# Kernel tuning notes

Measured on AMD Instinct MI355X. Metric: run time of the kernel, lower is better.

The kernel has to match this reference:

```python
import jax, jax.numpy as jnp
import numpy as np

T, B = 50, 512
S, A, BEL, H, E, M = 256, 32, 1024, 1024, 1024, 256
MIN_STD = 0.1


def setup_inputs() -> dict:
    key = jax.random.key(0)
    ks = jax.random.split(key, 24)
    def rn(k, shape, scale=1.0):
        return jax.random.normal(k, shape, dtype=jnp.float32) * scale
    w = 0.05  # weight init scale
    return {
        "prev_state": rn(ks[0], (B, S)),
        "actions": rn(ks[1], (T, B, A)),
        "prev_belief": rn(ks[2], (B, BEL)),
        "observations": rn(ks[3], (T, B, E)),
        "nonterminals": jnp.ones((T, B, 1), dtype=jnp.float32),
        "map_embeddings": rn(ks[4], (T, B, M)),
        "map_embeddings_post": rn(ks[5], (T, B, M)),
        "noise_prior": rn(ks[6], (T, B, S)),
        "noise_post": rn(ks[7], (T, B, S)),
        "W_sa": rn(ks[8], (BEL, S + A + M), w), "b_sa": jnp.zeros((BEL,), jnp.float32),
        "W_ih": rn(ks[9], (3 * BEL, BEL), w), "b_ih": jnp.zeros((3 * BEL,), jnp.float32),
        "W_hh": rn(ks[10], (3 * BEL, BEL), w), "b_hh": jnp.zeros((3 * BEL,), jnp.float32),
        "W_bp": rn(ks[11], (H, BEL), w), "b_bp": jnp.zeros((H,), jnp.float32),
        "W_sp": rn(ks[12], (2 * S, H), w), "b_sp": jnp.zeros((2 * S,), jnp.float32),
        "W_bq": rn(ks[13], (H, BEL + E + M), w), "b_bq": jnp.zeros((H,), jnp.float32),
        "W_sq": rn(ks[14], (2 * S, H), w), "b_sq": jnp.zeros((2 * S,), jnp.float32),
    }


def reference(prev_state, actions, prev_belief, observations, nonterminals,
              map_embeddings, map_embeddings_post, noise_prior, noise_post,
              W_sa, b_sa, W_ih, b_ih, W_hh, b_hh,
              W_bp, b_bp, W_sp, b_sp, W_bq, b_bq, W_sq, b_sq):
    relu = jax.nn.relu
    def lin(x, W, b):
        return x @ W.T + b

    def gru(x, h):  # torch.nn.GRUCell math
        gi = x @ W_ih.T + b_ih
        gh = h @ W_hh.T + b_hh
        i_r, i_z, i_n = jnp.split(gi, 3, axis=1)
        h_r, h_z, h_n = jnp.split(gh, 3, axis=1)
        r = jax.nn.sigmoid(i_r + h_r)
        z = jax.nn.sigmoid(i_z + h_z)
        n = jnp.tanh(i_n + r * h_n)
        return (1.0 - z) * n + z * h

    def std(raw):
        return jnp.minimum(jax.nn.softplus(raw) + MIN_STD, 5.0)

    def step(carry, xs):
        belief, post_state = carry
        a, obs, nt, me, mp, np_, nq = xs
        s = post_state * nt
        hid = relu(lin(jnp.concatenate([s, a, me], axis=1), W_sa, b_sa))
        belief = gru(hid, belief)
        # prior p(z_t | h_t)
        hp = relu(lin(belief, W_bp, b_bp))
        p_mean, p_raw = jnp.split(lin(hp, W_sp, b_sp), 2, axis=1)
        p_std = std(p_raw)
        p_state = p_mean + p_std * np_
        # posterior q(z_t | h_t, e_t, m_t)
        hq = relu(lin(jnp.concatenate([belief, obs, mp], axis=1), W_bq, b_bq))
        q_mean, q_raw = jnp.split(lin(hq, W_sq, b_sq), 2, axis=1)
        q_std = std(q_raw)
        q_state = q_mean + q_std * nq
        return (belief, q_state), (belief, p_state, p_mean, p_std, q_state, q_mean, q_std)

    _, outs = jax.lax.scan(
        step, (prev_belief, prev_state),
        (actions, observations, nonterminals, map_embeddings,
         map_embeddings_post, noise_prior, noise_post))
    return outs  # 7 arrays, each (T, B, *)
```

## Files before the change

### kernel.cpp

```cpp
#include <hip/hip_runtime.h>
#include <hip/hip_bf16.h>

#define NT 50
#define NB 512
#define SD 256
#define BD 1024
#define HD 1024
#define ED 1024
#define MD 256
#define NBLK 512
#define PGSZ (1024 * 256)
#define K1BIG 0x40000000

typedef __attribute__((ext_vector_type(8))) short bf16x8;
typedef __attribute__((ext_vector_type(4))) float f32x4;

__device__ __forceinline__ void gload_lds16(const void* g, void* l) {
  __builtin_amdgcn_global_load_lds(
      (const __attribute__((address_space(1))) void*)g,
      (__attribute__((address_space(3))) void*)l, 16, 0, 0);
}

__device__ __forceinline__ void aload16(const void* a, f32x4* r) {
  asm volatile("global_load_dwordx4 %0, %1, off sc0" : "=&v"(*r) : "v"(a) : "memory");
}
__device__ __forceinline__ void aload4(const void* a, float* r) {
  asm volatile("global_load_dword %0, %1, off sc0" : "=&v"(*r) : "v"(a) : "memory");
}
#define VMWAIT(N)                                        \
  asm volatile("s_waitcnt vmcnt(" #N ")" ::: "memory");  \
  __builtin_amdgcn_sched_barrier(0);

__device__ __forceinline__ void astore16(void* g, f32x4 v) {
  asm volatile("global_store_dwordx4 %0, %1, off sc0" :: "v"(g), "v"(v) : "memory");
}
__device__ __forceinline__ void astore4(void* g, float v) {
  asm volatile("global_store_dword %0, %1, off sc0" :: "v"(g), "v"(v) : "memory");
}
__device__ __forceinline__ void astore2(void* g, unsigned v) {
  asm volatile("global_store_short %0, %1, off sc0" :: "v"(g), "v"(v) : "memory");
}
__device__ __forceinline__ void ntstore16(void* g, f32x4 v) {
  asm volatile("global_store_dwordx4 %0, %1, off nt" :: "v"(g), "v"(v) : "memory");
}
__device__ __forceinline__ void ntstore4(void* g, float v) {
  asm volatile("global_store_dword %0, %1, off nt" :: "v"(g), "v"(v) : "memory");
}

__device__ __forceinline__ float sigmoidf_(float x) { return 1.0f / (1.0f + __expf(-x)); }
__device__ __forceinline__ float softplusf_(float x) {
  return (x > 0.0f) ? (x + log1pf(__expf(-x))) : log1pf(__expf(x));
}
__device__ __forceinline__ unsigned short bfb(float x) {
  __hip_bfloat16 h = __float2bfloat16(x);
  return __builtin_bit_cast(unsigned short, h);
}

__device__ __forceinline__ void xbar(unsigned* cnt, int inst, int xcd, int nx) {
  asm volatile("s_waitcnt vmcnt(0) lgkmcnt(0)" ::: "memory");
  __syncthreads();
  if (threadIdx.x == 0) {
    unsigned* c = cnt + 256 + (size_t)(inst * 8 + xcd) * 16;
    __hip_atomic_fetch_add(c, 1u, __ATOMIC_RELAXED, __HIP_MEMORY_SCOPE_AGENT);
    while (__hip_atomic_load(c, __ATOMIC_RELAXED, __HIP_MEMORY_SCOPE_AGENT) < (unsigned)nx)
      __builtin_amdgcn_s_sleep(4);
  }
  __syncthreads();
}

__device__ __noinline__ void gemm64(
    int EPI, char* lds,
    const __hip_bfloat16* __restrict__ A1, int lda1,
    const __hip_bfloat16* __restrict__ A2, int lda2, int K1,
    const __hip_bfloat16* __restrict__ Wr, int ldw, int nIter,
    const float* __restrict__ bias, const float* __restrict__ Cadd,
    float* __restrict__ Cf, __hip_bfloat16* __restrict__ Cb, int ldc, int m0) {
  const int tid = threadIdx.x;
  const int lane = tid & 63, w = tid >> 6;
  const int wr = w >> 1, wc = w & 1;
  f32x4 acc[2][2] = {};
  const __hip_bfloat16* a1r = A1 + (size_t)(m0 + lane) * lda1;
  const __hip_bfloat16* a2r = A2 ? (A2 + (size_t)(m0 + lane) * lda2) : a1r;
  const __hip_bfloat16* wrow = Wr + (size_t)lane * ldw;

  f32x4 rA0, rA1;
  auto issueA = [&](int it) {
    const int k0 = it << 6;
    const __hip_bfloat16* as = (k0 < K1) ? (a1r + k0) : (a2r + (k0 - K1));
    aload16(as + (2 * w) * 8, &rA0);
    aload16(as + (2 * w + 1) * 8, &rA1);
  };
  auto writeA = [&](int it) {
    char* la = lds + ((it & 1) << 14);
    *(f32x4*)(la + (2 * w) * 1024 + lane * 16) = rA0;
    *(f32x4*)(la + (2 * w + 1) * 1024 + lane * 16) = rA1;
  };
  auto stageW = [&](int it) {
    const int k0 = it << 6;
    char* lb = lds + ((it & 1) << 14) + 8192;
    gload_lds16(wrow + k0 + (2 * w) * 8, lb + (2 * w) * 1024);
    gload_lds16(wrow + k0 + (2 * w + 1) * 8, lb + (2 * w + 1) * 1024);
  };

  __syncthreads();
  issueA(0);
  VMWAIT(0)
  writeA(0);
  stageW(0);

  const int kq = lane >> 4, r15 = lane & 15;
  for (int i = 0; i < nIter; ++i) {
    __syncthreads();
    if (i + 1 < nIter) {
      issueA(i + 1);
      stageW(i + 1);
    }
    const char* la = lds + ((i & 1) << 14);
    const char* lb = la + 8192;
#pragma unroll
    for (int s = 0; s < 2; ++s) {
      bf16x8 af[2], bfr[2];
#pragma unroll
      for (int m = 0; m < 2; ++m)
        af[m] = *(const bf16x8*)(la + (size_t)((s * 4 + kq) * 64 + wr * 32 + m * 16 + r15) * 16);
#pragma unroll
      for (int n = 0; n < 2; ++n)
        bfr[n] = *(const bf16x8*)(lb + (size_t)((s * 4 + kq) * 64 + wc * 32 + n * 16 + r15) * 16);
#pragma unroll
      for (int m = 0; m < 2; ++m)
#pragma unroll
        for (int n = 0; n < 2; ++n)
          acc[m][n] = __builtin_amdgcn_mfma_f32_16x16x32_bf16(af[m], bfr[n], acc[m][n], 0, 0, 0);
    }
    if (i + 1 < nIter) {
      VMWAIT(2)
      writeA(i + 1);
    }
  }

  const int rg = lane >> 4;
  float ad[2][2][4];
  if (EPI == 3) {
#pragma unroll
    for (int m = 0; m < 2; ++m)
#pragma unroll
      for (int n = 0; n < 2; ++n) {
        const int col = wc * 32 + n * 16 + r15;
#pragma unroll
        for (int i2 = 0; i2 < 4; ++i2) {
          const int row = m0 + wr * 32 + m * 16 + rg * 4 + i2;
          aload4(Cadd + (size_t)row * ldc + col, &ad[m][n][i2]);
        }
      }
    VMWAIT(0)
  }
#pragma unroll
  for (int m = 0; m < 2; ++m) {
#pragma unroll
    for (int n = 0; n < 2; ++n) {
      const int col = wc * 32 + n * 16 + r15;
      const float bv = bias ? bias[col] : 0.0f;
#pragma unroll
      for (int i2 = 0; i2 < 4; ++i2) {
        const int row = m0 + wr * 32 + m * 16 + rg * 4 + i2;
        float v = acc[m][n][i2] + bv;
        if (EPI == 3) v += ad[m][n][i2];
        if (EPI != 0) {
          v = v > 0.0f ? v : 0.0f;
          astore2(Cb + (size_t)row * ldc + col, (unsigned)bfb(v));
        } else {
          astore4(Cf + (size_t)row * ldc + col, v);
        }
      }
    }
  }
}

__device__ __noinline__ void gemm_head64(
    char* lds, const __hip_bfloat16* __restrict__ A,
    const __hip_bfloat16* __restrict__ Wr, const float* __restrict__ bias,
    const float* __restrict__ noise, float* __restrict__ st_o, float* __restrict__ mn_o,
    float* __restrict__ sd_o, const float* __restrict__ ntn,
    __hip_bfloat16* __restrict__ sprev, int isq, int n0, int m0) {
  const int tid = threadIdx.x;
  const int lane = tid & 63, w = tid >> 6;
  const int wr = w >> 1, wc = w & 1;
  f32x4 acc[2][2] = {};
  const __hip_bfloat16* ar = A + (size_t)(m0 + lane) * BD;
  const __hip_bfloat16* wrow = Wr + (size_t)lane * BD;

  f32x4 rA0, rA1;
  auto issueA = [&](int it) {
    const int k0 = it << 6;
    aload16(ar + k0 + (2 * w) * 8, &rA0);
    aload16(ar + k0 + (2 * w + 1) * 8, &rA1);
  };
  auto writeA = [&](int it) {
    char* la = lds + ((it & 1) << 14);
    *(f32x4*)(la + (2 * w) * 1024 + lane * 16) = rA0;
    *(f32x4*)(la + (2 * w + 1) * 1024 + lane * 16) = rA1;
  };
  auto stageW = [&](int it) {
    const int k0 = it << 6;
    char* lb = lds + ((it & 1) << 14) + 8192;
    gload_lds16(wrow + k0 + (2 * w) * 8, lb + (2 * w) * 1024);
    gload_lds16(wrow + k0 + (2 * w + 1) * 8, lb + (2 * w + 1) * 1024);
  };

  __syncthreads();
  issueA(0);
  VMWAIT(0)
  writeA(0);
  stageW(0);

  const int kq = lane >> 4, r15 = lane & 15;
  for (int i = 0; i < 16; ++i) {
    __syncthreads();
    if (i + 1 < 16) {
      issueA(i + 1);
      stageW(i + 1);
    }
    const char* la = lds + ((i & 1) << 14);
    const char* lb = la + 8192;
#pragma unroll
    for (int s = 0; s < 2; ++s) {
      bf16x8 af[2], bfr[2];
#pragma unroll
      for (int m = 0; m < 2; ++m)
        af[m] = *(const bf16x8*)(la + (size_t)((s * 4 + kq) * 64 + wr * 32 + m * 16 + r15) * 16);
#pragma unroll
      for (int n = 0; n < 2; ++n)
        bfr[n] = *(const bf16x8*)(lb + (size_t)((s * 4 + kq) * 64 + wc * 32 + n * 16 + r15) * 16);
#pragma unroll
      for (int m = 0; m < 2; ++m)
#pragma unroll
        for (int n = 0; n < 2; ++n)
          acc[m][n] = __builtin_amdgcn_mfma_f32_16x16x32_bf16(af[m], bfr[n], acc[m][n], 0, 0, 0);
    }
    if (i + 1 < 16) {
      VMWAIT(2)
      writeA(i + 1);
    }
  }

  const int rg = lane >> 4;
  const bool even = (r15 & 1) == 0;
#pragma unroll
  for (int m = 0; m < 2; ++m) {
#pragma unroll
    for (int n = 0; n < 2; ++n) {
      const int col = n0 + wc * 32 + n * 16 + r15;
      const int j = col >> 1;
      const float bv = bias[col];
#pragma unroll
      for (int i2 = 0; i2 < 4; ++i2) {
        const int row = m0 + wr * 32 + m * 16 + rg * 4 + i2;
        float v = acc[m][n][i2] + bv;
        float partner = __shfl_xor(v, 1);
        float mean = even ? v : partner;
        float raw = even ? partner : v;
        float sd = fminf(softplusf_(raw) + 0.1f, 5.0f);
        const size_t o = (size_t)row * SD + j;
        if (even) {
          float st = mean + sd * noise[o];
          ntstore4(mn_o + o, mean);
          ntstore4(st_o + o, st);
          if (isq) astore2(sprev + o, (unsigned)bfb(st * ntn[row]));
        } else {
          ntstore4(sd_o + o, sd);
        }
      }
    }
  }
}

struct Args {
  const float *prev_state, *actions, *prev_belief, *observations, *nonterminals,
      *me, *mp, *noise_p, *noise_q,
      *W_sa, *b_sa, *W_ih, *b_ih, *W_hh, *b_hh,
      *W_bp, *b_bp, *W_sp, *b_sp, *W_bq, *b_bq, *W_sq, *b_sq;
  float* out;
  unsigned* cnt;
  __hip_bfloat16 *Wsa, *Wih, *Whh, *Wbp, *Wbq, *Wsp, *Wsq;
  __hip_bfloat16 *actme, *obsmp, *sprev, *bel, *hid, *hpb, *hqb;
  float *gi, *gh, *hq_obs;
  float *bsp_ro, *bsq_ro;
};

__global__ __launch_bounds__(256) void prep(Args P) {
  const int gtid = blockIdx.x * 256 + threadIdx.x;
  for (int i = gtid; i < BD * 576; i += PGSZ) {
    int r = i / 576, k = i - r * 576;
    P.Wsa[i] = __float2bfloat16(k < 544 ? P.W_sa[(size_t)r * 544 + k] : 0.0f);
  }
  for (int i = gtid; i < 3 * BD * BD; i += PGSZ) P.Wih[i] = __float2bfloat16(P.W_ih[i]);
  for (int i = gtid; i < 3 * BD * BD; i += PGSZ) P.Whh[i] = __float2bfloat16(P.W_hh[i]);
  for (int i = gtid; i < HD * BD; i += PGSZ) P.Wbp[i] = __float2bfloat16(P.W_bp[i]);
  for (int i = gtid; i < HD * 2304; i += PGSZ) P.Wbq[i] = __float2bfloat16(P.W_bq[i]);
  for (int i = gtid; i < 512 * HD; i += PGSZ) {
    int r = i >> 10, k = i & 1023;
    int dr = (r < 256) ? (2 * r) : (2 * (r - 256) + 1);
    P.Wsp[(size_t)dr * 1024 + k] = __float2bfloat16(P.W_sp[i]);
    P.Wsq[(size_t)dr * 1024 + k] = __float2bfloat16(P.W_sq[i]);
  }
  for (int i = gtid; i < 512; i += PGSZ) {
    int dr = (i < 256) ? (2 * i) : (2 * (i - 256) + 1);
    P.bsp_ro[dr] = P.b_sp[i];
    P.bsq_ro[dr] = P.b_sq[i];
  }
  for (int i = gtid; i < NT * NB * 320; i += PGSZ) {
    int tb = i / 320, j = i - tb * 320;
    float v = (j < 32) ? P.actions[(size_t)tb * 32 + j]
                       : (j < 288 ? P.me[(size_t)tb * 256 + (j - 32)] : 0.0f);
    P.actme[i] = __float2bfloat16(v);
  }
  for (int i = gtid; i < NB * 1280; i += PGSZ) {
    int bb = i / 1280, j = i - bb * 1280;
    float v = (j < ED) ? P.observations[(size_t)bb * ED + j] : P.mp[(size_t)bb * MD + (j - ED)];
    P.obsmp[i] = __float2bfloat16(v);
  }
  for (int i = gtid; i < NB * SD; i += PGSZ) {
    int r = i >> 8;
    P.sprev[i] = __float2bfloat16(P.prev_state[i] * P.nonterminals[r]);
  }
  for (int i = gtid; i < NB * BD; i += PGSZ) P.bel[i] = __float2bfloat16(P.prev_belief[i]);
}

__global__ __launch_bounds__(256, 4) void mega(Args P) {
  __shared__ alignas(16) char lds[32768];
  __shared__ int sh[3];
  const int tid = threadIdx.x;

  if (tid == 0) {
    unsigned x;
    asm volatile("s_getreg_b32 %0, hwreg(HW_REG_XCC_ID)" : "=s"(x));
    x &= 7u;
    unsigned s = __hip_atomic_fetch_add(P.cnt + x * 16, 1u, __ATOMIC_RELAXED,
                                        __HIP_MEMORY_SCOPE_AGENT);
    sh[0] = (int)x;
    sh[1] = (int)s;
  }
  __syncthreads();
  const int xcd = sh[0], slot = sh[1];

  if (tid == 0) {
    __hip_atomic_fetch_add(P.cnt + 128, 1u, __ATOMIC_RELAXED, __HIP_MEMORY_SCOPE_AGENT);
    while (__hip_atomic_load(P.cnt + 128, __ATOMIC_RELAXED, __HIP_MEMORY_SCOPE_AGENT) <
           (unsigned)NBLK)
      __builtin_amdgcn_s_sleep(4);
    sh[2] = (int)__hip_atomic_load(P.cnt + xcd * 16, __ATOMIC_RELAXED,
                                   __HIP_MEMORY_SCOPE_AGENT);
  }
  __syncthreads();
  const int nx = sh[2];
  const int m0 = xcd * 64;
  const size_t o_ps = (size_t)NT * NB * BD;
  const size_t blk = (size_t)NT * NB * SD;

  for (int t = 0; t < NT; ++t) {
    const int inst = t * 5;
    for (int tt = slot; tt < 64; tt += nx) {
      if (tt < 16) {
        const int n = tt;
        gemm64(1, lds, P.sprev, SD, P.actme + (size_t)t * NB * 320, 320, 256,
               P.Wsa + (size_t)n * 64 * 576, 576, 9,
               P.b_sa + n * 64, nullptr, nullptr, P.hid + n * 64, BD, m0);
      } else {
        const int n = tt - 16;
        gemm64(0, lds, P.bel, BD, nullptr, 0, K1BIG,
               P.Whh + (size_t)n * 64 * BD, BD, 16,
               P.b_hh + n * 64, nullptr, P.gh + n * 64, nullptr, 3 * BD, m0);
      }
    }
    xbar(P.cnt, inst + 0, xcd, nx);
    for (int tt = slot; tt < 64; tt += nx) {
      if (tt < 48) {
        const int n = tt;
        gemm64(0, lds, P.hid, BD, nullptr, 0, K1BIG,
               P.Wih + (size_t)n * 64 * BD, BD, 16,
               P.b_ih + n * 64, nullptr, P.gi + n * 64, nullptr, 3 * BD, m0);
      } else {
        const int n = tt - 48;
        gemm64(0, lds, P.obsmp, 1280, nullptr, 0, K1BIG,
               P.Wbq + (size_t)n * 64 * 2304 + 1024, 2304, 20,
               nullptr, nullptr, P.hq_obs + n * 64, nullptr, 1024, m0);
      }
    }
    xbar(P.cnt, inst + 1, xcd, nx);
    for (int u = slot * 256 + tid; u < 8192; u += nx * 256) {
      const int r = m0 + (u >> 7), j0 = (u & 127) << 3;
      const float* gib = P.gi + (size_t)r * 3072 + j0;
      const float* ghb = P.gh + (size_t)r * 3072 + j0;
      f32x4 ir0, ir1, iz0, iz1, in0, in1, hr0, hr1, hz0, hz1, hn0, hn1, hbv;
      aload16(gib, &ir0);
      aload16(gib + 4, &ir1);
      aload16(gib + 1024, &iz0);
      aload16(gib + 1028, &iz1);
      aload16(gib + 2048, &in0);
      aload16(gib + 2052, &in1);
      aload16(ghb, &hr0);
      aload16(ghb + 4, &hr1);
      aload16(ghb + 1024, &hz0);
      aload16(ghb + 1028, &hz1);
      aload16(ghb + 2048, &hn0);
      aload16(ghb + 2052, &hn1);
      aload16(P.bel + (size_t)r * BD + j0, &hbv);
      VMWAIT(0)
      bf16x8 hb = __builtin_bit_cast(bf16x8, hbv);
      float o[8];
      unsigned short nb[8];
#pragma unroll
      for (int k = 0; k < 8; ++k) {
        float gr = (k < 4 ? ir0[k] : ir1[k - 4]) + (k < 4 ? hr0[k] : hr1[k - 4]);
        float gz = (k < 4 ? iz0[k] : iz1[k - 4]) + (k < 4 ? hz0[k] : hz1[k - 4]);
        float hn = (k < 4 ? hn0[k] : hn1[k - 4]);
        float in_ = (k < 4 ? in0[k] : in1[k - 4]);
        float r_ = sigmoidf_(gr);
        float z_ = sigmoidf_(gz);
        float n_ = tanhf(in_ + r_ * hn);
        __hip_bfloat16 hv16 = __builtin_bit_cast(__hip_bfloat16, (unsigned short)hb[k]);
        float hv = __bfloat162float(hv16);
        float bel = (1.0f - z_) * n_ + z_ * hv;
        o[k] = bel;
        nb[k] = bfb(bel);
      }
      float* ob = P.out + (size_t)t * NB * BD + (size_t)r * BD + j0;
      ntstore16(ob, f32x4{o[0], o[1], o[2], o[3]});
      ntstore16(ob + 4, f32x4{o[4], o[5], o[6], o[7]});
      astore16(P.bel + (size_t)r * BD + j0, __builtin_bit_cast(f32x4, *(bf16x8*)nb));
    }
    if (t + 1 < NT) {
      for (int v = slot * 256 + tid; v < 5120; v += nx * 256) {
        const int r = m0 + v / 80, c0 = (v % 80) << 4;
        const float* src = (c0 < ED)
            ? (P.observations + (size_t)(t + 1) * NB * ED + (size_t)r * ED + c0)
            : (P.mp + (size_t)(t + 1) * NB * MD + (size_t)r * MD + (c0 - ED));
        unsigned short nb[16];
#pragma unroll
        for (int q = 0; q < 4; ++q) {
          f32x4 vv = *(const f32x4*)(src + q * 4);
#pragma unroll
          for (int kk = 0; kk < 4; ++kk) nb[q * 4 + kk] = bfb(vv[kk]);
        }
        astore16(P.obsmp + (size_t)r * 1280 + c0, __builtin_bit_cast(f32x4, *(bf16x8*)nb));
        astore16(P.obsmp + (size_t)r * 1280 + c0 + 8,
                 __builtin_bit_cast(f32x4, *(bf16x8*)(nb + 8)));
      }
    }
    xbar(P.cnt, inst + 2, xcd, nx);
    for (int tt = slot; tt < 32; tt += nx) {
      if (tt < 16) {
        const int n = tt;
        gemm64(1, lds, P.bel, BD, nullptr, 0, K1BIG,
               P.Wbp + (size_t)n * 64 * BD, BD, 16,
               P.b_bp + n * 64, nullptr, nullptr, P.hpb + n * 64, HD, m0);
      } else {
        const int n = tt - 16;
        gemm64(3, lds, P.bel, BD, nullptr, 0, K1BIG,
               P.Wbq + (size_t)n * 64 * 2304, 2304, 16,
               P.b_bq + n * 64, P.hq_obs + n * 64, nullptr, P.hqb + n * 64, HD, m0);
      }
    }
    xbar(P.cnt, inst + 3, xcd, nx);
    {
      const float* ntn = P.nonterminals + (size_t)((t + 1 < NT) ? t + 1 : t) * NB;
      const size_t to = (size_t)t * NB * SD;
      for (int tt = slot; tt < 16; tt += nx) {
        if (tt < 8)
          gemm_head64(lds, P.hpb, P.Wsp + (size_t)tt * 64 * BD, P.bsp_ro,
                      P.noise_p + to, P.out + o_ps + to, P.out + o_ps + blk + to,
                      P.out + o_ps + 2 * blk + to, ntn, P.sprev, 0, tt * 64, m0);
        else
          gemm_head64(lds, P.hqb, P.Wsq + (size_t)(tt - 8) * 64 * BD, P.bsq_ro,
                      P.noise_q + to, P.out + o_ps + 3 * blk + to,
                      P.out + o_ps + 4 * blk + to, P.out + o_ps + 5 * blk + to,
                      ntn, P.sprev, 1, (tt - 8) * 64, m0);
      }
    }
    xbar(P.cnt, inst + 4, xcd, nx);
  }
}


extern "C" void kernel_launch(void* const* d_in, const int* in_sizes, int n_in,
                              void* d_out, int out_size, void* d_ws, size_t ws_size,
                              hipStream_t stream) {
  Args P;
  P.prev_state = (const float*)d_in[0];
  P.actions = (const float*)d_in[1];
  P.prev_belief = (const float*)d_in[2];
  P.observations = (const float*)d_in[3];
  P.nonterminals = (const float*)d_in[4];
  P.me = (const float*)d_in[5];
  P.mp = (const float*)d_in[6];
  P.noise_p = (const float*)d_in[7];
  P.noise_q = (const float*)d_in[8];
  P.W_sa = (const float*)d_in[9];  P.b_sa = (const float*)d_in[10];
  P.W_ih = (const float*)d_in[11]; P.b_ih = (const float*)d_in[12];
  P.W_hh = (const float*)d_in[13]; P.b_hh = (const float*)d_in[14];
  P.W_bp = (const float*)d_in[15]; P.b_bp = (const float*)d_in[16];
  P.W_sp = (const float*)d_in[17]; P.b_sp = (const float*)d_in[18];
  P.W_bq = (const float*)d_in[19]; P.b_bq = (const float*)d_in[20];
  P.W_sq = (const float*)d_in[21]; P.b_sq = (const float*)d_in[22];
  P.out = (float*)d_out;

  char* p = (char*)d_ws;
  auto carve = [&](size_t bytes) -> char* {
    char* r = p;
    p += (bytes + 255) & ~(size_t)255;
    return r;
  };
  const size_t cnt_bytes = (size_t)65536 * 4;
  P.cnt = (unsigned*)carve(cnt_bytes);
  P.Wsa = (__hip_bfloat16*)carve((size_t)BD * 576 * 2);
  P.Wih = (__hip_bfloat16*)carve((size_t)3 * BD * BD * 2);
  P.Whh = (__hip_bfloat16*)carve((size_t)3 * BD * BD * 2);
  P.Wbp = (__hip_bfloat16*)carve((size_t)HD * BD * 2);
  P.Wbq = (__hip_bfloat16*)carve((size_t)HD * 2304 * 2);
  P.Wsp = (__hip_bfloat16*)carve((size_t)512 * HD * 2);
  P.Wsq = (__hip_bfloat16*)carve((size_t)512 * HD * 2);
  P.bsp_ro = (float*)carve(512 * 4);
  P.bsq_ro = (float*)carve(512 * 4);
  P.actme = (__hip_bfloat16*)carve((size_t)NT * NB * 320 * 2);
  P.obsmp = (__hip_bfloat16*)carve((size_t)NB * 1280 * 2);
  P.sprev = (__hip_bfloat16*)carve((size_t)NB * SD * 2);
  P.bel = (__hip_bfloat16*)carve((size_t)NB * BD * 2);
  P.hid = (__hip_bfloat16*)carve((size_t)NB * BD * 2);
  P.hpb = (__hip_bfloat16*)carve((size_t)NB * HD * 2);
  P.hqb = (__hip_bfloat16*)carve((size_t)NB * HD * 2);
  P.gi = (float*)carve((size_t)NB * 3 * BD * 4);
  P.gh = (float*)carve((size_t)NB * 3 * BD * 4);
  P.hq_obs = (float*)carve((size_t)NB * HD * 4);

  hipMemsetAsync(P.cnt, 0, cnt_bytes, stream);
  prep<<<1024, 256, 0, stream>>>(P);
  mega<<<NBLK, 256, 0, stream>>>(P);
}
```

Before: 5.488 ms.

## Triple-buffer GEMM tiles with direct global-to-LDS loads for activations

Both GEMM routines now load the activation tile straight into LDS with global_load_lds (sc0 cache bit) instead of going through registers, and use a three-slot LDS ring with two stages of prefetch. Only one barrier is taken per K-step, after a partial vmcnt wait. This is meant to hide global load latency better and remove the register round-trip and the extra __syncthreads. In exchange LDS per block grows to 48KB and the launch-bounds occupancy hint drops from 4 to 2. The spin-barrier sleep is also shortened.

New measurement: 5.311 ms. -3.2%, faster.

```diff
diff --git a/kernel.cpp b/kernel.cpp
--- a/kernel.cpp
+++ b/kernel.cpp
@@ -20,6 +20,11 @@
       (const __attribute__((address_space(1))) void*)g,
       (__attribute__((address_space(3))) void*)l, 16, 0, 0);
 }
+__device__ __forceinline__ void gload_lds16_sc0(const void* g, void* l) {
+  __builtin_amdgcn_global_load_lds(
+      (const __attribute__((address_space(1))) void*)g,
+      (__attribute__((address_space(3))) void*)l, 16, 0, 1);
+}
 
 __device__ __forceinline__ void aload16(const void* a, f32x4* r) {
   asm volatile("global_load_dwordx4 %0, %1, off sc0" : "=&v"(*r) : "v"(a) : "memory");
@@ -63,7 +68,7 @@
     unsigned* c = cnt + 256 + (size_t)(inst * 8 + xcd) * 16;
     __hip_atomic_fetch_add(c, 1u, __ATOMIC_RELAXED, __HIP_MEMORY_SCOPE_AGENT);
     while (__hip_atomic_load(c, __ATOMIC_RELAXED, __HIP_MEMORY_SCOPE_AGENT) < (unsigned)nx)
-      __builtin_amdgcn_s_sleep(4);
+      __builtin_amdgcn_s_sleep(2);
   }
   __syncthreads();
 }
@@ -83,39 +88,28 @@
   const __hip_bfloat16* a2r = A2 ? (A2 + (size_t)(m0 + lane) * lda2) : a1r;
   const __hip_bfloat16* wrow = Wr + (size_t)lane * ldw;
 
-  f32x4 rA0, rA1;
-  auto issueA = [&](int it) {
+  auto stage = [&](int it) {
     const int k0 = it << 6;
+    char* la = lds + (size_t)(it % 3) * 16384;
+    char* lb = la + 8192;
     const __hip_bfloat16* as = (k0 < K1) ? (a1r + k0) : (a2r + (k0 - K1));
-    aload16(as + (2 * w) * 8, &rA0);
-    aload16(as + (2 * w + 1) * 8, &rA1);
-  };
-  auto writeA = [&](int it) {
-    char* la = lds + ((it & 1) << 14);
-    *(f32x4*)(la + (2 * w) * 1024 + lane * 16) = rA0;
-    *(f32x4*)(la + (2 * w + 1) * 1024 + lane * 16) = rA1;
-  };
-  auto stageW = [&](int it) {
-    const int k0 = it << 6;
-    char* lb = lds + ((it & 1) << 14) + 8192;
+    gload_lds16_sc0(as + (2 * w) * 8, la + (2 * w) * 1024);
+    gload_lds16_sc0(as + (2 * w + 1) * 8, la + (2 * w + 1) * 1024);
     gload_lds16(wrow + k0 + (2 * w) * 8, lb + (2 * w) * 1024);
     gload_lds16(wrow + k0 + (2 * w + 1) * 8, lb + (2 * w + 1) * 1024);
   };
 
   __syncthreads();
-  issueA(0);
-  VMWAIT(0)
-  writeA(0);
-  stageW(0);
+  stage(0);
+  stage(1);
+  VMWAIT(4)
+  __builtin_amdgcn_s_barrier();
+  __builtin_amdgcn_sched_barrier(0);
 
   const int kq = lane >> 4, r15 = lane & 15;
   for (int i = 0; i < nIter; ++i) {
-    __syncthreads();
-    if (i + 1 < nIter) {
-      issueA(i + 1);
-      stageW(i + 1);
-    }
-    const char* la = lds + ((i & 1) << 14);
+    if (i + 2 < nIter) stage(i + 2);
+    const char* la = lds + (size_t)(i % 3) * 16384;
     const char* lb = la + 8192;
 #pragma unroll
     for (int s = 0; s < 2; ++s) {
@@ -133,8 +127,13 @@
           acc[m][n] = __builtin_amdgcn_mfma_f32_16x16x32_bf16(af[m], bfr[n], acc[m][n], 0, 0, 0);
     }
     if (i + 1 < nIter) {
-      VMWAIT(2)
-      writeA(i + 1);
+      if (i + 2 < nIter) {
+        VMWAIT(4)
+      } else {
+        VMWAIT(0)
+      }
+      __builtin_amdgcn_s_barrier();
+      __builtin_amdgcn_sched_barrier(0);
     }
   }
 
@@ -189,38 +188,27 @@
   const __hip_bfloat16* ar = A + (size_t)(m0 + lane) * BD;
   const __hip_bfloat16* wrow = Wr + (size_t)lane * BD;
 
-  f32x4 rA0, rA1;
-  auto issueA = [&](int it) {
+  auto stage = [&](int it) {
     const int k0 = it << 6;
-    aload16(ar + k0 + (2 * w) * 8, &rA0);
-    aload16(ar + k0 + (2 * w + 1) * 8, &rA1);
-  };
-  auto writeA = [&](int it) {
-    char* la = lds + ((it & 1) << 14);
-    *(f32x4*)(la + (2 * w) * 1024 + lane * 16) = rA0;
-    *(f32x4*)(la + (2 * w + 1) * 1024 + lane * 16) = rA1;
-  };
-  auto stageW = [&](int it) {
-    const int k0 = it << 6;
-    char* lb = lds + ((it & 1) << 14) + 8192;
+    char* la = lds + (size_t)(it % 3) * 16384;
+    char* lb = la + 8192;
+    gload_lds16_sc0(ar + k0 + (2 * w) * 8, la + (2 * w) * 1024);
+    gload_lds16_sc0(ar + k0 + (2 * w + 1) * 8, la + (2 * w + 1) * 1024);
     gload_lds16(wrow + k0 + (2 * w) * 8, lb + (2 * w) * 1024);
     gload_lds16(wrow + k0 + (2 * w + 1) * 8, lb + (2 * w + 1) * 1024);
   };
 
   __syncthreads();
-  issueA(0);
-  VMWAIT(0)
-  writeA(0);
-  stageW(0);
+  stage(0);
+  stage(1);
+  VMWAIT(4)
+  __builtin_amdgcn_s_barrier();
+  __builtin_amdgcn_sched_barrier(0);
 
   const int kq = lane >> 4, r15 = lane & 15;
   for (int i = 0; i < 16; ++i) {
-    __syncthreads();
-    if (i + 1 < 16) {
-      issueA(i + 1);
-      stageW(i + 1);
-    }
-    const char* la = lds + ((i & 1) << 14);
+    if (i + 2 < 16) stage(i + 2);
+    const char* la = lds + (size_t)(i % 3) * 16384;
     const char* lb = la + 8192;
 #pragma unroll
     for (int s = 0; s < 2; ++s) {
@@ -238,8 +226,13 @@
           acc[m][n] = __builtin_amdgcn_mfma_f32_16x16x32_bf16(af[m], bfr[n], acc[m][n], 0, 0, 0);
     }
     if (i + 1 < 16) {
-      VMWAIT(2)
-      writeA(i + 1);
+      if (i + 2 < 16) {
+        VMWAIT(4)
+      } else {
+        VMWAIT(0)
+      }
+      __builtin_amdgcn_s_barrier();
+      __builtin_amdgcn_sched_barrier(0);
     }
   }
 
@@ -326,8 +319,8 @@
   for (int i = gtid; i < NB * BD; i += PGSZ) P.bel[i] = __float2bfloat16(P.prev_belief[i]);
 }
 
-__global__ __launch_bounds__(256, 4) void mega(Args P) {
-  __shared__ alignas(16) char lds[32768];
+__global__ __launch_bounds__(256, 2) void mega(Args P) {
+  __shared__ alignas(16) char lds[49152];
   __shared__ int sh[3];
   const int tid = threadIdx.x;
 
```
